# Optimization experiments

Hardware: AMD Instinct MI355X
Metric: run time of the kernel (lower is better)

## Reference

```python
import jax, jax.numpy as jnp
import numpy as np

N_VARS = 16
BATCH = 16
SEQ = 512
P = N_VARS * (N_VARS - 1)  # ordered pairs i != j


def setup_inputs() -> dict:
    key = jax.random.key(0)
    ks = jax.random.split(key, 12)
    n = N_VARS

    def w(k, shape, fan_in):
        return jax.random.normal(k, shape, dtype=jnp.float32) / np.sqrt(fan_in)

    z = lambda *s: jnp.zeros(s, jnp.float32)
    return {
        'data': jax.random.normal(ks[0], (BATCH, SEQ, n), dtype=jnp.float32),
        # structure learner: n*n -> 256 -> 128 -> n*n (dropout skipped / eval mode)
        'Ws1': w(ks[1], (n * n, 256), n * n), 'bs1': z(256),
        'Ws2': w(ks[2], (256, 128), 256), 'bs2': z(128),
        'Ws3': w(ks[3], (128, n * n), 128), 'bs3': z(n * n),
        # per-variable causal mechanisms (stacked): (n-1) -> 128 -> 64 -> 1
        'Wm1': w(ks[4], (n, n - 1, 128), n - 1), 'bm1': z(n, 128),
        'Wm2': w(ks[5], (n, 128, 64), 128), 'bm2': z(n, 64),
        'Wm3': w(ks[6], (n, 64), 64), 'bm3': z(n),
        # per-pair independence tests (stacked): 2 -> 32 -> 1, sigmoid
        'Wt1': w(ks[7], (P, 2, 32), 2), 'bt1': z(P, 32),
        'Wt2': w(ks[8], (P, 32), 32), 'bt2': z(P),
    }


def reference(data, Ws1, bs1, Ws2, bs2, Ws3, bs3,
              Wm1, bm1, Wm2, bm2, Wm3, bm3,
              Wt1, bt1, Wt2, bt2):
    B, S, n = data.shape
    N = B * S
    flat = data.reshape(N, n)  # [N, n] all samples

    # ---- correlations of batch-averaged series (vectorized corrcoef) ----
    avg = data.mean(axis=0)                    # [S, n]
    xc = avg - avg.mean(axis=0, keepdims=True)
    cov = xc.T @ xc                            # [n, n]
    std = jnp.sqrt(jnp.clip(jnp.diag(cov), 0.0))
    denom = std[:, None] * std[None, :]
    corr = jnp.abs(jnp.where(denom > 0, cov / jnp.where(denom > 0, denom, 1.0), 0.0))
    corr = corr * (1.0 - jnp.eye(n, dtype=corr.dtype))  # zero diagonal (i != j only)

    # ---- structure learner MLP -> sigmoid -> strict upper-tri DAG mask ----
    h = jax.nn.relu(corr.reshape(1, -1) @ Ws1 + bs1)
    h = jax.nn.relu(h @ Ws2 + bs2)
    adj = jax.nn.sigmoid(h @ Ws3 + bs3).reshape(n, n)
    adj = jnp.triu(adj, 1)

    # ---- causal mechanisms: gather-parents -> per-var MLP -> scatter ----
    idx = np.stack([[j for j in range(n) if j != v] for v in range(n)])  # [n, n-1]
    pmask = adj > 0.5
    parent_mask = pmask[idx, np.arange(n)[:, None]].astype(flat.dtype)   # [n, n-1]
    inp = flat[:, idx] * parent_mask[None]                               # [N, n, n-1]
    h1 = jax.nn.relu(jnp.einsum('nvp,vph->nvh', inp, Wm1) + bm1)         # [N, n, 128]
    h2 = jax.nn.relu(jnp.einsum('nvh,vhk->nvk', h1, Wm2) + bm2)          # [N, n, 64]
    mech = jnp.einsum('nvk,vk->nv', h2, Wm3) + bm3                       # [N, n]
    has_parents = parent_mask.sum(axis=1) > 0                            # [n]
    predictions = jnp.where(has_parents[None, :], mech, flat).reshape(B, S, n)

    # ---- batched per-pair independence tests ----
    pairs = np.array([(i, j) for i in range(n) for j in range(n) if i != j])
    pi, pj = pairs[:, 0], pairs[:, 1]
    X = jnp.stack([flat[:, pi], flat[:, pj]], axis=-1)                   # [N, P, 2]
    ht = jax.nn.relu(jnp.einsum('npc,pch->nph', X, Wt1) + bt1)           # [N, P, 32]
    s = jax.nn.sigmoid(jnp.einsum('nph,ph->np', ht, Wt2) + bt2).mean(axis=0)  # [P]
    scores = jnp.zeros((n, n), flat.dtype).at[pi, pj].set(s)

    return adj, predictions, scores
```

## Files before the change

kernel.cpp:

```cpp
#include <hip/hip_runtime.h>
#include <hip/hip_bf16.h>


typedef __attribute__((ext_vector_type(8))) short bf16x8;
typedef __attribute__((ext_vector_type(4))) short bf16x4;
typedef __attribute__((ext_vector_type(4))) float f32x4;

#define DEV __device__ __forceinline__
DEV short f2bf(float f){ __hip_bfloat16 h = __float2bfloat16(f); short s; __builtin_memcpy(&s,&h,2); return s; }

struct GraphSm {
    float avT[16 * 532];
    float part[512];
    float cov[256];
    float corr[256];
    float h1[256];
    float h2[128];
    float adj[256];
    float m[16];
    float stdv[16];
};
struct MechSm {
    short W2T[64 * 136];
    short H1[8][16 * 136];
    float W1[16 * 128];
    float B1[128];
    float B2[64];
    float W3[64];
};
struct PairSm {
    float w0[32], w1[32], bb[32], w2[32];
    float red[512];
    float b2s;
};
union SmU { GraphSm g; MechSm m; PairSm p; };

__global__ void __launch_bounds__(512, 2) k_fused(
    const float* __restrict__ data,
    const float* __restrict__ Ws1, const float* __restrict__ bs1,
    const float* __restrict__ Ws2, const float* __restrict__ bs2,
    const float* __restrict__ Ws3, const float* __restrict__ bs3,
    const float* __restrict__ Wm1, const float* __restrict__ bm1,
    const float* __restrict__ Wm2, const float* __restrict__ bm2,
    const float* __restrict__ Wm3, const float* __restrict__ bm3,
    const float* __restrict__ Wt1, const float* __restrict__ bt1,
    const float* __restrict__ Wt2, const float* __restrict__ bt2,
    float* __restrict__ out)
{
    __shared__ __align__(16) SmU sm;
    __shared__ float pm_s[16];
    __shared__ float hp_s;
    int tid = threadIdx.x, bid = blockIdx.x;

    if (bid >= 128) {
        int p = bid - 128;
        int i = p / 15, jr = p % 15;
        int j = jr + (jr >= i ? 1 : 0);
        if (tid < 32) {
            sm.p.w0[tid] = Wt1[p*64 + tid];
            sm.p.w1[tid] = Wt1[p*64 + 32 + tid];
            sm.p.bb[tid] = bt1[p*32 + tid];
            sm.p.w2[tid] = Wt2[p*32 + tid];
        }
        if (tid == 0) sm.p.b2s = bt2[p];
        __syncthreads();
        float b2sv = sm.p.b2s;
        float acc = 0.f;
        float nxa = data[tid*16 + i];
        float nxb = data[tid*16 + j];
        for (int it = 0; it < 16; ++it) {
            float xa = nxa, xb = nxb;
            if (it < 15) {
                int sn = (it+1)*512 + tid;
                nxa = data[sn*16 + i];
                nxb = data[sn*16 + j];
            }
            float za = 0.f, zb = 0.f;
            #pragma unroll
            for (int h = 0; h < 32; h += 2) {
                float t1 = fmaf(xa, sm.p.w0[h],   fmaf(xb, sm.p.w1[h],   sm.p.bb[h]));
                za = fmaf(fmaxf(t1, 0.f), sm.p.w2[h],   za);
                float t2 = fmaf(xa, sm.p.w0[h+1], fmaf(xb, sm.p.w1[h+1], sm.p.bb[h+1]));
                zb = fmaf(fmaxf(t2, 0.f), sm.p.w2[h+1], zb);
            }
            float z = b2sv + za + zb;
            acc += __builtin_amdgcn_rcpf(1.f + __expf(-z));
        }
        sm.p.red[tid] = acc;
        __syncthreads();
        for (int off = 256; off > 0; off >>= 1) {
            if (tid < off) sm.p.red[tid] += sm.p.red[tid + off];
            __syncthreads();
        }
        if (tid == 0) out[256 + 131072 + i*16 + j] = sm.p.red[0] * (1.f/8192.f);
        return;
    }

    int v = bid >> 3, chunk = bid & 7;
    int gs0 = chunk * 1024;

    {
        int vb = (tid & 3) * 4, sg = tid >> 2;
        for (int k = 0; k < 4; ++k) {
            int s = sg + k*128;
            float ax=0.f, ay=0.f, az=0.f, aw=0.f;
            #pragma unroll
            for (int b = 0; b < 16; ++b) {
                float4 d4 = *(const float4*)&data[b*8192 + s*16 + vb];
                ax += d4.x; ay += d4.y; az += d4.z; aw += d4.w;
            }
            sm.g.avT[(vb+0)*532 + s] = ax * 0.0625f;
            sm.g.avT[(vb+1)*532 + s] = ay * 0.0625f;
            sm.g.avT[(vb+2)*532 + s] = az * 0.0625f;
            sm.g.avT[(vb+3)*532 + s] = aw * 0.0625f;
        }
    }
    __syncthreads();
    if (tid < 128) {
        int vv = tid >> 3, sgm = tid & 7;
        const float* rp = &sm.g.avT[vv*532 + sgm*64];
        float a0=0.f, a1=0.f, a2=0.f, a3=0.f;
        for (int s = 0; s < 64; s += 4) {
            float4 fa = *(const float4*)&rp[s];
            a0 += fa.x; a1 += fa.y; a2 += fa.z; a3 += fa.w;
        }
        sm.g.part[tid] = (a0+a1)+(a2+a3);
    }
    __syncthreads();
    if (tid < 16) {
        float ms = 0.f;
        #pragma unroll
        for (int q = 0; q < 8; ++q) ms += sm.g.part[tid*8 + q];
        sm.g.m[tid] = ms * (1.f/512.f);
    }
    __syncthreads();
    {
        int t = tid & 255, hh = tid >> 8;
        int ci = t >> 4, cj = t & 15;
        const float* pi_ = &sm.g.avT[ci*532 + hh*256];
        const float* pj_ = &sm.g.avT[cj*532 + hh*256];
        float a0=0.f, a1=0.f, a2=0.f, a3=0.f;
        #pragma unroll 8
        for (int s = 0; s < 256; s += 4) {
            float4 fa = *(const float4*)&pi_[s];
            float4 fb = *(const float4*)&pj_[s];
            a0 = fmaf(fa.x, fb.x, a0); a1 = fmaf(fa.y, fb.y, a1);
            a2 = fmaf(fa.z, fb.z, a2); a3 = fmaf(fa.w, fb.w, a3);
        }
        sm.g.part[tid] = (a0+a1)+(a2+a3);
    }
    __syncthreads();
    if (tid < 256) {
        int ci = tid >> 4, cj = tid & 15;
        sm.g.cov[tid] = sm.g.part[tid] + sm.g.part[256 + tid]
                      - 512.f * sm.g.m[ci] * sm.g.m[cj];
    }
    __syncthreads();
    if (tid < 16) sm.g.stdv[tid] = sqrtf(fmaxf(sm.g.cov[tid*17], 0.f));
    __syncthreads();
    if (tid < 256) {
        int ci = tid >> 4, cj = tid & 15;
        float den = sm.g.stdv[ci] * sm.g.stdv[cj];
        sm.g.corr[tid] = (den > 0.f && ci != cj) ? fabsf(sm.g.cov[tid]/den) : 0.f;
    }
    __syncthreads();

    float* red2 = sm.g.avT;

    {
        int o4 = tid & 63, ks = tid >> 6;
        const float* W1p = Ws1 + ks*32*256 + o4*4;
        const float* cp  = sm.g.corr + ks*32;
        float ax=0.f, ay=0.f, az=0.f, aw=0.f;
        float bx=0.f, by=0.f, bz=0.f, bw=0.f;
        #pragma unroll 8
        for (int i = 0; i < 32; i += 2) {
            float4 w0 = *(const float4*)&W1p[(i  )*256];
            float4 w1 = *(const float4*)&W1p[(i+1)*256];
            float c0 = cp[i], c1 = cp[i+1];
            ax=fmaf(c0,w0.x,ax); ay=fmaf(c0,w0.y,ay); az=fmaf(c0,w0.z,az); aw=fmaf(c0,w0.w,aw);
            bx=fmaf(c1,w1.x,bx); by=fmaf(c1,w1.y,by); bz=fmaf(c1,w1.z,bz); bw=fmaf(c1,w1.w,bw);
        }
        float4 r4; r4.x=ax+bx; r4.y=ay+by; r4.z=az+bz; r4.w=aw+bw;
        *(float4*)&red2[ks*256 + o4*4] = r4;
    }
    __syncthreads();
    if (tid < 256) {
        float s = bs1[tid];
        #pragma unroll
        for (int k2 = 0; k2 < 8; ++k2) s += red2[k2*256 + tid];
        sm.g.h1[tid] = fmaxf(s, 0.f);
    }
    __syncthreads();
    {
        int o4 = tid & 31, ks = tid >> 5;
        const float* W2p = Ws2 + ks*16*128 + o4*4;
        const float* cp  = sm.g.h1 + ks*16;
        float ax=0.f, ay=0.f, az=0.f, aw=0.f;
        float bx=0.f, by=0.f, bz=0.f, bw=0.f;
        #pragma unroll
        for (int i = 0; i < 16; i += 2) {
            float4 w0 = *(const float4*)&W2p[(i  )*128];
            float4 w1 = *(const float4*)&W2p[(i+1)*128];
            float c0 = cp[i], c1 = cp[i+1];
            ax=fmaf(c0,w0.x,ax); ay=fmaf(c0,w0.y,ay); az=fmaf(c0,w0.z,az); aw=fmaf(c0,w0.w,aw);
            bx=fmaf(c1,w1.x,bx); by=fmaf(c1,w1.y,by); bz=fmaf(c1,w1.z,bz); bw=fmaf(c1,w1.w,bw);
        }
        float4 r4; r4.x=ax+bx; r4.y=ay+by; r4.z=az+bz; r4.w=aw+bw;
        *(float4*)&red2[ks*128 + o4*4] = r4;
    }
    __syncthreads();
    if (tid < 128) {
        float s = bs2[tid];
        #pragma unroll
        for (int k2 = 0; k2 < 16; ++k2) s += red2[k2*128 + tid];
        sm.g.h2[tid] = fmaxf(s, 0.f);
    }
    __syncthreads();
    {
        int o4 = tid & 63, ks = tid >> 6;
        const float* W3p = Ws3 + ks*16*256 + o4*4;
        const float* cp  = sm.g.h2 + ks*16;
        float ax=0.f, ay=0.f, az=0.f, aw=0.f;
        float bx=0.f, by=0.f, bz=0.f, bw=0.f;
        #pragma unroll
        for (int i = 0; i < 16; i += 2) {
            float4 w0 = *(const float4*)&W3p[(i  )*256];
            float4 w1 = *(const float4*)&W3p[(i+1)*256];
            float c0 = cp[i], c1 = cp[i+1];
            ax=fmaf(c0,w0.x,ax); ay=fmaf(c0,w0.y,ay); az=fmaf(c0,w0.z,az); aw=fmaf(c0,w0.w,aw);
            bx=fmaf(c1,w1.x,bx); by=fmaf(c1,w1.y,by); bz=fmaf(c1,w1.z,bz); bw=fmaf(c1,w1.w,bw);
        }
        float4 r4; r4.x=ax+bx; r4.y=ay+by; r4.z=az+bz; r4.w=aw+bw;
        *(float4*)&red2[ks*256 + o4*4] = r4;
    }
    __syncthreads();
    if (tid < 256) {
        float z = bs3[tid];
        #pragma unroll
        for (int k2 = 0; k2 < 8; ++k2) z += red2[k2*256 + tid];
        float a = 1.f / (1.f + expf(-z));
        int r = tid >> 4, cc = tid & 15;
        float adjv = (r < cc) ? a : 0.f;
        sm.g.adj[tid] = adjv;
        if (bid == 0) out[tid] = adjv;
    }
    __syncthreads();
    if (tid < 15) {
        int jj = tid + (tid >= v ? 1 : 0);
        pm_s[tid] = (sm.g.adj[jj*16 + v] > 0.5f) ? 1.f : 0.f;
    }
    if (bid == 0 && tid >= 16 && tid < 32)
        out[256 + 131072 + (tid-16)*17] = 0.f;
    __syncthreads();
    if (tid == 0) {
        float s = 0.f;
        #pragma unroll
        for (int pr = 0; pr < 15; ++pr) s += pm_s[pr];
        hp_s = (s > 0.f) ? 1.f : 0.f;
    }
    __syncthreads();

    for (int e = tid; e < 2048; e += 512) {
        int k = e >> 7, h = e & 127;
        float val = 0.f;
        if (k != v) {
            int p = k - (k > v ? 1 : 0);
            val = Wm1[v*1920 + p*128 + h] * pm_s[p];
        }
        sm.m.W1[e] = val;
    }
    for (int e = tid; e < 8192; e += 512) {
        int h = e >> 6, jj2 = e & 63;
        sm.m.W2T[jj2*136 + h] = f2bf(Wm2[v*8192 + e]);
    }
    if (tid < 128) sm.m.B1[tid] = bm1[v*128 + tid];
    else if (tid < 192) sm.m.B2[tid - 128] = bm2[v*64 + tid - 128];
    else if (tid < 256) sm.m.W3[tid - 192] = Wm3[v*64 + tid - 192];
    __syncthreads();

    int lane = tid & 63, wid = tid >> 6;
    int c = lane & 15, q = lane >> 4;
    float hp = hp_s;
    float bm3v = bm3[v];

    bf16x8 a1f[8];
    #pragma unroll
    for (int ht = 0; ht < 8; ++ht) {
        #pragma unroll
        for (int jj = 0; jj < 8; ++jj) {
            int k = q*8 + jj;
            float w = (k < 16) ? sm.m.W1[k*128 + ht*16 + c] : 0.f;
            a1f[ht][jj] = f2bf(w);
        }
    }
    bf16x8 b2r[16];
    #pragma unroll
    for (int jt = 0; jt < 4; ++jt)
        #pragma unroll
        for (int ks = 0; ks < 4; ++ks)
            b2r[jt*4 + ks] = *(const bf16x8*)&sm.m.W2T[(jt*16 + c)*136 + ks*32 + q*8];
    float w3c[4], b2c[4];
    #pragma unroll
    for (int jt = 0; jt < 4; ++jt) { w3c[jt] = sm.m.W3[jt*16 + c]; b2c[jt] = sm.m.B2[jt*16 + c]; }

    short* h1buf = sm.m.H1[wid];
    bool act = (q < 2);

    float4 u0c, u1c;
    {
        int st0 = wid*8;
        if (act) {
            const float* xp = &data[(gs0 + st0*16 + c)*16 + q*8];
            u0c = *(const float4*)xp;
            u1c = *(const float4*)(xp + 4);
        }
    }

    for (int stl = 0; stl < 8; ++stl) {
        int st = wid*8 + stl;
        float4 u0 = u0c, u1 = u1c;
        if (stl < 7 && act) {
            const float* xp = &data[(gs0 + (st+1)*16 + c)*16 + q*8];
            u0c = *(const float4*)xp;
            u1c = *(const float4*)(xp + 4);
        }
        bf16x8 xb;
        #pragma unroll
        for (int i2 = 0; i2 < 8; ++i2) xb[i2] = 0;
        if (act) {
            xb[0] = f2bf(u0.x); xb[1] = f2bf(u0.y);
            xb[2] = f2bf(u0.z); xb[3] = f2bf(u0.w);
            xb[4] = f2bf(u1.x); xb[5] = f2bf(u1.y);
            xb[6] = f2bf(u1.z); xb[7] = f2bf(u1.w);
        }
        f32x4 c1[8];
        #pragma unroll
        for (int ht = 0; ht < 8; ++ht) c1[ht] = *(const f32x4*)&sm.m.B1[ht*16 + q*4];
        #pragma unroll
        for (int ht = 0; ht < 8; ++ht)
            c1[ht] = __builtin_amdgcn_mfma_f32_16x16x32_bf16(a1f[ht], xb, c1[ht], 0, 0, 0);
        #pragma unroll
        for (int ht = 0; ht < 8; ++ht) {
            bf16x4 pk;
            #pragma unroll
            for (int r = 0; r < 4; ++r) pk[r] = f2bf(fmaxf(c1[ht][r], 0.f));
            *(bf16x4*)&h1buf[c*136 + ht*16 + q*4] = pk;
        }
        f32x4 c2[4];
        #pragma unroll
        for (int jt = 0; jt < 4; ++jt) {
            float bi = b2c[jt];
            c2[jt] = (f32x4){bi, bi, bi, bi};
        }
        #pragma unroll
        for (int ks = 0; ks < 4; ++ks) {
            bf16x8 a2 = *(const bf16x8*)&h1buf[c*136 + ks*32 + q*8];
            #pragma unroll
            for (int jt = 0; jt < 4; ++jt)
                c2[jt] = __builtin_amdgcn_mfma_f32_16x16x32_bf16(a2, b2r[jt*4 + ks], c2[jt], 0, 0, 0);
        }
        float part[4];
        #pragma unroll
        for (int r = 0; r < 4; ++r) part[r] = 0.f;
        #pragma unroll
        for (int jt = 0; jt < 4; ++jt)
            #pragma unroll
            for (int r = 0; r < 4; ++r)
                part[r] = fmaf(fmaxf(c2[jt][r], 0.f), w3c[jt], part[r]);
        #pragma unroll
        for (int off = 1; off < 16; off <<= 1)
            #pragma unroll
            for (int r = 0; r < 4; ++r)
                part[r] += __shfl_xor(part[r], off, 16);
        if (c == 0) {
            #pragma unroll
            for (int r = 0; r < 4; ++r) {
                int s_loc = st*16 + q*4 + r;
                float mech = part[r] + bm3v;
                float xv = data[(gs0 + s_loc)*16 + v];
                out[256 + (gs0 + s_loc)*16 + v] = (hp != 0.f) ? mech : xv;
            }
        }
    }
}

extern "C" void kernel_launch(void* const* d_in, const int* in_sizes, int n_in,
                              void* d_out, int out_size, void* d_ws, size_t ws_size,
                              hipStream_t stream)
{
    const float* data = (const float*)d_in[0];
    const float* Ws1  = (const float*)d_in[1];
    const float* bs1  = (const float*)d_in[2];
    const float* Ws2  = (const float*)d_in[3];
    const float* bs2  = (const float*)d_in[4];
    const float* Ws3  = (const float*)d_in[5];
    const float* bs3  = (const float*)d_in[6];
    const float* Wm1  = (const float*)d_in[7];
    const float* bm1  = (const float*)d_in[8];
    const float* Wm2  = (const float*)d_in[9];
    const float* bm2  = (const float*)d_in[10];
    const float* Wm3  = (const float*)d_in[11];
    const float* bm3  = (const float*)d_in[12];
    const float* Wt1  = (const float*)d_in[13];
    const float* bt1  = (const float*)d_in[14];
    const float* Wt2  = (const float*)d_in[15];
    const float* bt2  = (const float*)d_in[16];
    float* out = (float*)d_out;
    (void)d_ws; (void)ws_size; (void)in_sizes; (void)n_in; (void)out_size;

    hipLaunchKernelGGL(k_fused, dim3(368), dim3(512), 0, stream,
                       data, Ws1, bs1, Ws2, bs2, Ws3, bs3,
                       Wm1, bm1, Wm2, bm2, Wm3, bm3,
                       Wt1, bt1, Wt2, bt2, out);
}
```

Measured before the change: 117.7 us.

## Prefetch mechanism weights into registers early and collapse graph-stage barriers

Loads the per-variable mechanism weights and biases (Wm1, Wm2, bm1, bm2, Wm3, structure-MLP biases) into registers at kernel start, so their global latency overlaps the correlation and structure-MLP phases. It also removes several __syncthreads rounds by having each thread compute means, diagonal covariances and the parent mask redundantly instead of staging them through shared memory. The cost is higher register pressure, with launch bounds at 512 threads and 2 blocks per CU, and some redundant shared-memory reads. The Wm2 transpose store pattern changes to 16 contiguous elements per thread, which may cause more LDS bank conflicts.

```diff
diff --git a/kernel.cpp b/kernel.cpp
--- a/kernel.cpp
+++ b/kernel.cpp
@@ -12,13 +12,10 @@
 struct GraphSm {
     float avT[16 * 532];
     float part[512];
-    float cov[256];
     float corr[256];
     float h1[256];
     float h2[128];
     float adj[256];
-    float m[16];
-    float stdv[16];
 };
 struct MechSm {
     short W2T[64 * 136];
@@ -48,8 +45,6 @@
     float* __restrict__ out)
 {
     __shared__ __align__(16) SmU sm;
-    __shared__ float pm_s[16];
-    __shared__ float hp_s;
     int tid = threadIdx.x, bid = blockIdx.x;
 
     if (bid >= 128) {
@@ -99,6 +94,33 @@
     int v = bid >> 3, chunk = bid & 7;
     int gs0 = chunk * 1024;
 
+    float pf_wm1[4];
+    {
+        #pragma unroll
+        for (int r = 0; r < 4; ++r) {
+            int e = tid + 512*r;
+            int k = e >> 7, h = e & 127;
+            pf_wm1[r] = 0.f;
+            if (k != v) {
+                int p = k - (k > v ? 1 : 0);
+                pf_wm1[r] = Wm1[v*1920 + p*128 + h];
+            }
+        }
+    }
+    float4 pf_wm2[4];
+    {
+        const float* wp = Wm2 + v*8192 + tid*16;
+        #pragma unroll
+        for (int m4 = 0; m4 < 4; ++m4) pf_wm2[m4] = *(const float4*)&wp[m4*4];
+    }
+    float b1r  = bm1[v*128 + (tid & 127)];
+    float b2r_ = bm2[v*64  + (tid & 63)];
+    float w3r  = Wm3[v*64  + (tid & 63)];
+    float bm3v = bm3[v];
+    float bs1r = bs1[tid & 255];
+    float bs2r = bs2[tid & 127];
+    float bs3r = bs3[tid & 255];
+
     {
         int vb = (tid & 3) * 4, sg = tid >> 2;
         for (int k = 0; k < 4; ++k) {
@@ -124,19 +146,17 @@
             float4 fa = *(const float4*)&rp[s];
             a0 += fa.x; a1 += fa.y; a2 += fa.z; a3 += fa.w;
         }
-        sm.g.part[tid] = (a0+a1)+(a2+a3);
-    }
-    __syncthreads();
-    if (tid < 16) {
-        float ms = 0.f;
-        #pragma unroll
-        for (int q = 0; q < 8; ++q) ms += sm.g.part[tid*8 + q];
-        sm.g.m[tid] = ms * (1.f/512.f);
-    }
-    __syncthreads();
+        sm.g.h2[tid] = (a0+a1)+(a2+a3);
+    }
+    __syncthreads();
+    int ci, cj; float mci, mcj;
     {
         int t = tid & 255, hh = tid >> 8;
-        int ci = t >> 4, cj = t & 15;
+        ci = t >> 4; cj = t & 15;
+        mci = 0.f; mcj = 0.f;
+        #pragma unroll
+        for (int q = 0; q < 8; ++q) { mci += sm.g.h2[ci*8 + q]; mcj += sm.g.h2[cj*8 + q]; }
+        mci *= (1.f/512.f); mcj *= (1.f/512.f);
         const float* pi_ = &sm.g.avT[ci*532 + hh*256];
         const float* pj_ = &sm.g.avT[cj*532 + hh*256];
         float a0=0.f, a1=0.f, a2=0.f, a3=0.f;
@@ -151,17 +171,11 @@
     }
     __syncthreads();
     if (tid < 256) {
-        int ci = tid >> 4, cj = tid & 15;
-        sm.g.cov[tid] = sm.g.part[tid] + sm.g.part[256 + tid]
-                      - 512.f * sm.g.m[ci] * sm.g.m[cj];
-    }
-    __syncthreads();
-    if (tid < 16) sm.g.stdv[tid] = sqrtf(fmaxf(sm.g.cov[tid*17], 0.f));
-    __syncthreads();
-    if (tid < 256) {
-        int ci = tid >> 4, cj = tid & 15;
-        float den = sm.g.stdv[ci] * sm.g.stdv[cj];
-        sm.g.corr[tid] = (den > 0.f && ci != cj) ? fabsf(sm.g.cov[tid]/den) : 0.f;
+        float cij = sm.g.part[tid] + sm.g.part[256 + tid] - 512.f*mci*mcj;
+        float cii = sm.g.part[ci*17] + sm.g.part[256 + ci*17] - 512.f*mci*mci;
+        float cjj = sm.g.part[cj*17] + sm.g.part[256 + cj*17] - 512.f*mcj*mcj;
+        float den = sqrtf(fmaxf(cii, 0.f)) * sqrtf(fmaxf(cjj, 0.f));
+        sm.g.corr[tid] = (den > 0.f && ci != cj) ? fabsf(cij/den) : 0.f;
     }
     __syncthreads();
 
@@ -186,7 +200,7 @@
     }
     __syncthreads();
     if (tid < 256) {
-        float s = bs1[tid];
+        float s = bs1r;
         #pragma unroll
         for (int k2 = 0; k2 < 8; ++k2) s += red2[k2*256 + tid];
         sm.g.h1[tid] = fmaxf(s, 0.f);
@@ -211,7 +225,7 @@
     }
     __syncthreads();
     if (tid < 128) {
-        float s = bs2[tid];
+        float s = bs2r;
         #pragma unroll
         for (int k2 = 0; k2 < 16; ++k2) s += red2[k2*128 + tid];
         sm.g.h2[tid] = fmaxf(s, 0.f);
@@ -236,7 +250,7 @@
     }
     __syncthreads();
     if (tid < 256) {
-        float z = bs3[tid];
+        float z = bs3r;
         #pragma unroll
         for (int k2 = 0; k2 < 8; ++k2) z += red2[k2*256 + tid];
         float a = 1.f / (1.f + expf(-z));
@@ -245,44 +259,40 @@
         sm.g.adj[tid] = adjv;
         if (bid == 0) out[tid] = adjv;
     }
-    __syncthreads();
-    if (tid < 15) {
-        int jj = tid + (tid >= v ? 1 : 0);
-        pm_s[tid] = (sm.g.adj[jj*16 + v] > 0.5f) ? 1.f : 0.f;
-    }
-    if (bid == 0 && tid >= 16 && tid < 32)
-        out[256 + 131072 + (tid-16)*17] = 0.f;
-    __syncthreads();
-    if (tid == 0) {
-        float s = 0.f;
-        #pragma unroll
-        for (int pr = 0; pr < 15; ++pr) s += pm_s[pr];
-        hp_s = (s > 0.f) ? 1.f : 0.f;
-    }
-    __syncthreads();
-
-    for (int e = tid; e < 2048; e += 512) {
-        int k = e >> 7, h = e & 127;
+    if (bid == 0 && tid >= 256 && tid < 272)
+        out[256 + 131072 + (tid-256)*17] = 0.f;
+    __syncthreads();
+
+    #pragma unroll
+    for (int r = 0; r < 4; ++r) {
+        int e = tid + 512*r;
+        int k = e >> 7;
         float val = 0.f;
-        if (k != v) {
-            int p = k - (k > v ? 1 : 0);
-            val = Wm1[v*1920 + p*128 + h] * pm_s[p];
-        }
+        if (k != v && sm.g.adj[k*16 + v] > 0.5f) val = pf_wm1[r];
         sm.m.W1[e] = val;
     }
-    for (int e = tid; e < 8192; e += 512) {
-        int h = e >> 6, jj2 = e & 63;
-        sm.m.W2T[jj2*136 + h] = f2bf(Wm2[v*8192 + e]);
-    }
-    if (tid < 128) sm.m.B1[tid] = bm1[v*128 + tid];
-    else if (tid < 192) sm.m.B2[tid - 128] = bm2[v*64 + tid - 128];
-    else if (tid < 256) sm.m.W3[tid - 192] = Wm3[v*64 + tid - 192];
+    float hp = 0.f;
+    #pragma unroll
+    for (int k = 0; k < 16; ++k)
+        if (k != v && sm.g.adj[k*16 + v] > 0.5f) hp = 1.f;
+    #pragma unroll
+    for (int m4 = 0; m4 < 4; ++m4) {
+        float4 w4 = pf_wm2[m4];
+        int e0 = tid*16 + m4*4;
+        int h = e0 >> 6;
+        int jj0 = e0 & 63;
+        sm.m.W2T[(jj0+0)*136 + h] = f2bf(w4.x);
+        sm.m.W2T[(jj0+1)*136 + h] = f2bf(w4.y);
+        sm.m.W2T[(jj0+2)*136 + h] = f2bf(w4.z);
+        sm.m.W2T[(jj0+3)*136 + h] = f2bf(w4.w);
+    }
+    if (tid < 128) sm.m.B1[tid] = b1r;
+    else if (tid < 192) sm.m.B2[tid - 128] = b2r_;
+    else if (tid < 256) sm.m.W3[tid - 192] = w3r;
     __syncthreads();
 
     int lane = tid & 63, wid = tid >> 6;
     int c = lane & 15, q = lane >> 4;
-    float hp = hp_s;
-    float bm3v = bm3[v];
 
     bf16x8 a1f[8];
     #pragma unroll
```

Measured after the change: 115.5 us. No clear change (-1.9%).
